# Optimization experiments

Hardware: AMD Instinct MI355X
Metric: run time of the kernel (lower is better)

Reference implementation:

```python
import jax, jax.numpy as jnp
import numpy as np

N, D, K, A, BINS, DEPTH = 1024, 384, 64, 5, 64, 4
D_MAX = 22.0


def _expected_distance(distogram):
    # distance_one_hot_inverse(softmax(distogram), 0.0, 22.0, 64)
    step = D_MAX / BINS
    centers = step * jnp.arange(BINS, dtype=distogram.dtype) + step / 2
    p = jax.nn.softmax(distogram, axis=-1)  # [N,N,BINS]
    return (p * centers).sum(axis=-1)       # [N,N]


def _extract_neighbours(pos, prev_pos, distogram, resi, chain, batch, mask, key):
    inf = jnp.inf
    same_batch = batch[:, None] == batch[None, :]
    same_chain = (chain[:, None] == chain[None, :]) & same_batch
    pair_mask = mask[:, None] & mask[None, :] & same_batch
    # sequence-separation distance (only within a chain), 3.81 A per residue
    seq_d = jnp.where(same_chain,
                      jnp.abs(resi[:, None] - resi[None, :]).astype(jnp.float32) * 3.81,
                      inf)
    md = _expected_distance(distogram)
    d = jnp.minimum(seq_d, jnp.where(md < 8.0, md, inf))
    ca = pos[:, 1]                                   # current CA positions [N,3]
    d = jnp.minimum(d, jnp.linalg.norm(ca[:, None] - ca[None, :], axis=-1))
    pca = prev_pos[:, 1]
    d = jnp.minimum(d, jnp.linalg.norm(pca[:, None] - pca[None, :], axis=-1))
    d = jnp.where(same_batch, d, inf)
    log_p = -3.0 * d
    u = jax.random.uniform(key, d.shape)
    gumbel = -jnp.log(-jnp.log(u + 1e-6) + 1e-6)
    random_distance = -(log_p + gumbel)
    random_distance = jnp.where(pair_mask, random_distance, inf)
    neg_vals, idx = jax.lax.top_k(-random_distance, K)  # k smallest random distances
    nbr_mask = jnp.isfinite(neg_vals)                   # invalid neighbours have -inf
    return idx, nbr_mask                                # [N,K] int32, [N,K] bool


def setup_inputs() -> dict:
    key = jax.random.key(0)
    ks = jax.random.split(key, 8)
    local = jax.random.normal(ks[0], (N, D), dtype=jnp.float32)
    pos = 3.0 * jax.random.normal(ks[1], (N, A, 3), dtype=jnp.float32)
    prev_pos = 3.0 * jax.random.normal(ks[2], (N, A, 3), dtype=jnp.float32)
    distogram = jax.random.normal(ks[3], (N, N, BINS), dtype=jnp.float32)
    Wn = jax.random.normal(ks[4], (D, D), dtype=jnp.float32) / np.sqrt(D)
    Wp = 0.01 * jax.random.normal(ks[5], (D, A * 3), dtype=jnp.float32)
    ar = jnp.arange(N, dtype=jnp.int32)
    batch = ar // 256          # 4 proteins of 256 residues
    chain = (ar // 128) % 2    # 2 chains per protein
    resi = ar % 128            # residue index within chain
    mask = jnp.ones((N,), dtype=bool)
    return {"local": local, "pos": pos, "prev_pos": prev_pos, "distogram": distogram,
            "Wn": Wn, "Wp": Wp, "resi": resi, "chain": chain, "batch": batch, "mask": mask}


def reference(local, pos, prev_pos, distogram, Wn, Wp, resi, chain, batch, mask):
    mask_f = mask.astype(local.dtype)
    key = jax.random.key(42)
    traj = []
    for t in range(DEPTH):  # diffusion_depth iterations, neighbours recomputed each block
        idx, nbr_mask = _extract_neighbours(pos, prev_pos, distogram, resi, chain,
                                            batch, mask, jax.random.fold_in(key, t))
        nf = local[idx] * nbr_mask[..., None].astype(local.dtype)   # [N,K,D]
        cnt = jnp.maximum(nbr_mask.sum(axis=1, keepdims=True).astype(local.dtype), 1.0)
        msg = nf.sum(axis=1) / cnt                                   # [N,D]
        local = local + jax.nn.gelu(msg @ Wn)
        pos = pos + 0.1 * (local @ Wp).reshape(N, A, 3) * mask_f[:, None, None]
        traj.append(pos)
    trajectory = jnp.stack(traj)  # [DEPTH,N,A,3]
    return local, pos, trajectory
```

## Files before the change

kernel.cpp:

```cpp
#include <hip/hip_runtime.h>
#include <stdint.h>

typedef unsigned int u32;
typedef unsigned long long u64;

#define NN 1024
#define DDIM 384
#define KNB 64
#define BINS_ 64
#define DEPTH_ 4

#define OUT_POS 393216
#define OUT_TRAJ 408576

__device__ __forceinline__ u32 rotl32(u32 x, int r) { return (x << r) | (x >> (32 - r)); }

__device__ __forceinline__ void threefry(u32 k0, u32 k1, u32 x0, u32 x1, u32& o0, u32& o1) {
  u32 ks2 = k0 ^ k1 ^ 0x1BD11BDAu;
#define TF_R(r) { x0 += x1; x1 = rotl32(x1, r); x1 ^= x0; }
  x0 += k0; x1 += k1;
  TF_R(13) TF_R(15) TF_R(26) TF_R(6)
  x0 += k1; x1 += ks2 + 1u;
  TF_R(17) TF_R(29) TF_R(16) TF_R(24)
  x0 += ks2; x1 += k0 + 2u;
  TF_R(13) TF_R(15) TF_R(26) TF_R(6)
  x0 += k0; x1 += k1 + 3u;
  TF_R(17) TF_R(29) TF_R(16) TF_R(24)
  x0 += k1; x1 += ks2 + 4u;
  TF_R(13) TF_R(15) TF_R(26) TF_R(6)
  x0 += ks2; x1 += k0 + 5u;
#undef TF_R
  o0 = x0; o1 = x1;
}

static inline u32 h_rotl32(u32 x, int r) { return (x << r) | (x >> (32 - r)); }
static void h_threefry(u32 k0, u32 k1, u32 x0, u32 x1, u32& o0, u32& o1) {
  u32 ks2 = k0 ^ k1 ^ 0x1BD11BDAu;
#define TF_R(r) { x0 += x1; x1 = h_rotl32(x1, r); x1 ^= x0; }
  x0 += k0; x1 += k1;
  TF_R(13) TF_R(15) TF_R(26) TF_R(6)
  x0 += k1; x1 += ks2 + 1u;
  TF_R(17) TF_R(29) TF_R(16) TF_R(24)
  x0 += ks2; x1 += k0 + 2u;
  TF_R(13) TF_R(15) TF_R(26) TF_R(6)
  x0 += k0; x1 += k1 + 3u;
  TF_R(17) TF_R(29) TF_R(16) TF_R(24)
  x0 += k1; x1 += ks2 + 4u;
  TF_R(13) TF_R(15) TF_R(26) TF_R(6)
  x0 += ks2; x1 += k0 + 5u;
#undef TF_R
  o0 = x0; o1 = x1;
}

__global__ __launch_bounds__(256) void k_dstatic(
    const float* __restrict__ disto, const float* __restrict__ ppos,
    const int* __restrict__ resi, const int* __restrict__ chain,
    const int* __restrict__ batch, float* __restrict__ dstat) {
  int p = blockIdx.x * 256 + threadIdx.x;
  int i = p >> 10, j = p & 1023;
  if (batch[i] != batch[j]) { dstat[p] = __builtin_inff(); return; }
  float seq_d = __builtin_inff();
  if (chain[i] == chain[j]) {
    int dr = resi[i] - resi[j];
    seq_d = __fmul_rn(fabsf((float)dr), 3.81f);
  }
  const float4* dp = reinterpret_cast<const float4*>(disto + (size_t)p * BINS_);
  float w[BINS_];
#pragma unroll
  for (int q = 0; q < 16; ++q) {
    float4 v = dp[q];
    w[4*q+0] = v.x; w[4*q+1] = v.y; w[4*q+2] = v.z; w[4*q+3] = v.w;
  }
  float m = -__builtin_inff();
#pragma unroll
  for (int q = 0; q < BINS_; ++q) m = fmaxf(m, w[q]);
  float s = 0.f;
#pragma unroll
  for (int q = 0; q < BINS_; ++q) {
    w[q] = expf(__fsub_rn(w[q], m));
    s = __fadd_rn(s, w[q]);
  }
  float e = 0.f;
#pragma unroll
  for (int q = 0; q < BINS_; ++q) {
    float pq = __fdiv_rn(w[q], s);
    e = __fadd_rn(e, __fmul_rn(pq, 0.34375f * (float)q + 0.171875f));
  }
  float md = e;
  float d = fminf(seq_d, (md < 8.0f) ? md : __builtin_inff());
  float ax = __fsub_rn(ppos[i*15+3], ppos[j*15+3]);
  float ay = __fsub_rn(ppos[i*15+4], ppos[j*15+4]);
  float az = __fsub_rn(ppos[i*15+5], ppos[j*15+5]);
  float ss = __fadd_rn(__fadd_rn(__fmul_rn(ax,ax), __fmul_rn(ay,ay)), __fmul_rn(az,az));
  dstat[p] = fminf(d, __fsqrt_rn(ss));
}

__device__ __forceinline__ u64 shx64(u64 x, int m) {
  int lo = __shfl_xor((int)(u32)x, m, 64);
  int hi = __shfl_xor((int)(u32)(x >> 32), m, 64);
  return ((u64)(u32)hi << 32) | (u32)lo;
}

__device__ __forceinline__ u64 merge64(u64 a, u64 b, int lane) {
  u64 br = shx64(b, 63);
  u64 m = (a < br) ? a : br;
  for (int stride = 32; stride > 0; stride >>= 1) {
    u64 p = shx64(m, stride);
    u64 lo = (m < p) ? m : p;
    u64 hi = (m < p) ? p : m;
    m = ((lane & stride) == 0) ? lo : hi;
  }
  return m;
}

__global__ __launch_bounds__(384) void k_round(
    const float* __restrict__ dstat, const float* __restrict__ Lprev,
    float* __restrict__ Lnext, const float* __restrict__ posP,
    float* __restrict__ posN, const int* __restrict__ batch,
    const float* __restrict__ Wn, const float* __restrict__ Wp,
    float* __restrict__ out, int t, u32 fk0, u32 fk1) {
  __shared__ int sidx[4][KNB];
  __shared__ float cntL[4];
  __shared__ float msgT[4][DDIM];
  __shared__ float lrT[4][DDIM + 1];
  const int tid = threadIdx.x;
  const int w = tid >> 6, lane = tid & 63;
  const int i0 = blockIdx.x * 4;

  if (w < 4) {
    const int i = i0 + w;
    const int bi = batch[i];
    const float cax = posP[i*15+3], cay = posP[i*15+4], caz = posP[i*15+5];
    u64 v[16];
#pragma unroll
    for (int c = 0; c < 16; ++c) {
      int j = c*64 + lane;
      float rd = __builtin_inff();
      if (batch[j] == bi) {
        float d = dstat[i*NN + j];
        float dx = __fsub_rn(cax, posP[j*15+3]);
        float dy = __fsub_rn(cay, posP[j*15+4]);
        float dz = __fsub_rn(caz, posP[j*15+5]);
        float ss = __fadd_rn(__fadd_rn(__fmul_rn(dx,dx), __fmul_rn(dy,dy)), __fmul_rn(dz,dz));
        d = fminf(d, __fsqrt_rn(ss));
        u32 o0, o1;
        threefry(fk0, fk1, 0u, (u32)(i*NN + j), o0, o1);
        u32 bits = o0 ^ o1;
        float u = __fsub_rn(__uint_as_float((bits >> 9) | 0x3f800000u), 1.0f);
        float inner = __fadd_rn(-logf(__fadd_rn(u, 1e-6f)), 1e-6f);
        float gum = -logf(inner);
        float logp = __fmul_rn(-3.0f, d);
        rd = -__fadd_rn(logp, gum);
      }
      u32 fb = __float_as_uint(rd);
      u32 km = (fb & 0x80000000u) ? ~fb : (fb | 0x80000000u);
      v[c] = ((u64)km << 32) | (u32)j;
    }
    for (int size = 2; size <= 64; size <<= 1) {
      for (int stride = size >> 1; stride > 0; stride >>= 1) {
        bool keepmin = (((lane & stride) == 0) == ((lane & size) == 0));
#pragma unroll
        for (int c = 0; c < 16; ++c) {
          u64 p = shx64(v[c], stride);
          u64 lo = (v[c] < p) ? v[c] : p;
          u64 hi = (v[c] < p) ? p : v[c];
          v[c] = keepmin ? lo : hi;
        }
      }
    }
#pragma unroll
    for (int c = 0; c < 8; ++c) v[c] = merge64(v[2*c], v[2*c+1], lane);
#pragma unroll
    for (int c = 0; c < 4; ++c) v[c] = merge64(v[2*c], v[2*c+1], lane);
#pragma unroll
    for (int c = 0; c < 2; ++c) v[c] = merge64(v[2*c], v[2*c+1], lane);
    u64 m = merge64(v[0], v[1], lane);
    u32 km = (u32)(m >> 32);
    bool fin = (km < 0xFF800000u);
    sidx[w][lane] = fin ? (int)(u32)(m & 0xffffffffu) : -1;
    u64 ball = __ballot(fin);
    if (lane == 0) cntL[w] = fmaxf((float)__popcll(ball), 1.0f);
  }
  __syncthreads();

  {
    const int c = tid;
#pragma unroll
    for (int r = 0; r < 4; ++r) {
      float s = 0.f;
#pragma unroll 8
      for (int k = 0; k < KNB; ++k) {
        int id = sidx[r][k];
        if (id >= 0) s += Lprev[id*DDIM + c];
      }
      msgT[r][c] = s / cntL[r];
    }
  }
  __syncthreads();

  {
    const int c = tid;
    float a0 = 0.f, a1 = 0.f, a2 = 0.f, a3 = 0.f;
#pragma unroll 8
    for (int dd = 0; dd < DDIM; ++dd) {
      float wv = Wn[dd*DDIM + c];
      a0 = fmaf(msgT[0][dd], wv, a0);
      a1 = fmaf(msgT[1][dd], wv, a1);
      a2 = fmaf(msgT[2][dd], wv, a2);
      a3 = fmaf(msgT[3][dd], wv, a3);
    }
    float accs[4] = {a0, a1, a2, a3};
#pragma unroll
    for (int r = 0; r < 4; ++r) {
      float x = accs[r];
      float th = tanhf(0.7978845608028654f * (x + 0.044715f * x * x * x));
      float g = 0.5f * x * (1.0f + th);
      float ln = Lprev[(i0 + r)*DDIM + c] + g;
      Lnext[(i0 + r)*DDIM + c] = ln;
      lrT[r][c] = ln;
    }
  }
  __syncthreads();

  if (tid < 60) {
    const int r = tid / 15, cc = tid % 15;
    const int i = i0 + r;
    float acc = 0.f;
#pragma unroll 8
    for (int dd = 0; dd < DDIM; ++dd) acc = fmaf(lrT[r][dd], Wp[dd*15 + cc], acc);
    float pv = posP[i*15 + cc] + 0.1f * acc;
    posN[i*15 + cc] = pv;
    out[OUT_TRAJ + t*15360 + i*15 + cc] = pv;
  }
}

extern "C" void kernel_launch(void* const* d_in, const int* in_sizes, int n_in,
                              void* d_out, int out_size, void* d_ws, size_t ws_size,
                              hipStream_t stream) {
  (void)in_sizes; (void)n_in; (void)out_size; (void)ws_size;
  const float* local_in = (const float*)d_in[0];
  const float* pos_in   = (const float*)d_in[1];
  const float* ppos_in  = (const float*)d_in[2];
  const float* disto    = (const float*)d_in[3];
  const float* Wn       = (const float*)d_in[4];
  const float* Wp       = (const float*)d_in[5];
  const int* resi       = (const int*)d_in[6];
  const int* chain      = (const int*)d_in[7];
  const int* batch      = (const int*)d_in[8];
  float* out = (float*)d_out;
  char* ws = (char*)d_ws;
  float* dstat = (float*)(ws + 0);
  float* L0    = (float*)(ws + 4194304);
  float* L1    = (float*)(ws + 5767168);
  float* P0    = (float*)(ws + 7340032);
  float* P1    = (float*)(ws + 7401472);

  k_dstatic<<<dim3(4096), dim3(256), 0, stream>>>(disto, ppos_in, resi, chain, batch, dstat);

  const float* Lp = local_in;
  const float* Pp = pos_in;
  float* Lbuf[2] = {L0, L1};
  float* Pbuf[2] = {P0, P1};
  for (int t = 0; t < DEPTH_; ++t) {
    u32 fk0, fk1;
    h_threefry(0u, 42u, 0u, (u32)t, fk0, fk1);
    float* Ln = (t == DEPTH_ - 1) ? out : Lbuf[t & 1];
    float* Pn = (t == DEPTH_ - 1) ? (out + OUT_POS) : Pbuf[t & 1];
    k_round<<<dim3(256), dim3(384), 0, stream>>>(dstat, Lp, Ln, Pp, Pn, batch,
                                                 Wn, Wp, out, t, fk0, fk1);
    Lp = Ln; Pp = Pn;
  }
}
```

Measured before the change: 687.8 us.

## Split top-k selection from gather/matmul and skip sorting chunks outside the batch

Each round is split into two kernels. A one-wave-per-row top-k kernel runs on 1024 blocks and skips the bitonic sort and merges for 64-column chunks that hold no same-batch entries. A separate gather/matmul/update kernel then handles 2 rows per block across 512 blocks. The aim is more parallelism than the previous 256 blocks, where only 4 of 6 waves did the top-k, and less wasted sorting of all-infinite chunks. The cost is an extra launch per round and an index/count round trip through global memory, and each Wn column is now loaded for 2 rows instead of 4.

```diff
diff --git a/kernel.cpp b/kernel.cpp
--- a/kernel.cpp
+++ b/kernel.cpp
@@ -101,6 +101,19 @@
   return ((u64)(u32)hi << 32) | (u32)lo;
 }
 
+__device__ __forceinline__ u64 sort64(u64 x, int lane) {
+  for (int size = 2; size <= 64; size <<= 1) {
+    for (int stride = size >> 1; stride > 0; stride >>= 1) {
+      bool keepmin = (((lane & stride) == 0) == ((lane & size) == 0));
+      u64 p = shx64(x, stride);
+      u64 lo = (x < p) ? x : p;
+      u64 hi = (x < p) ? p : x;
+      x = keepmin ? lo : hi;
+    }
+  }
+  return x;
+}
+
 __device__ __forceinline__ u64 merge64(u64 a, u64 b, int lane) {
   u64 br = shx64(b, 63);
   u64 m = (a < br) ? a : br;
@@ -113,105 +126,129 @@
   return m;
 }
 
-__global__ __launch_bounds__(384) void k_round(
-    const float* __restrict__ dstat, const float* __restrict__ Lprev,
-    float* __restrict__ Lnext, const float* __restrict__ posP,
-    float* __restrict__ posN, const int* __restrict__ batch,
+__global__ __launch_bounds__(64) void k_topk(
+    const float* __restrict__ dstat, const float* __restrict__ posP,
+    const int* __restrict__ batch, int* __restrict__ idx,
+    float* __restrict__ cntv, u32 fk0, u32 fk1) {
+  const int i = blockIdx.x;
+  const int lane = threadIdx.x;
+  const int bi = batch[i];
+  const float cax = posP[i*15+3], cay = posP[i*15+4], caz = posP[i*15+5];
+  u64 v[16];
+  unsigned vmask = 0;
+#pragma unroll
+  for (int c = 0; c < 16; ++c) {
+    int j = c*64 + lane;
+    bool sb = (batch[j] == bi);
+    if (__ballot(sb) != 0ull) vmask |= (1u << c);
+    float rd = __builtin_inff();
+    if (sb) {
+      float d = dstat[i*NN + j];
+      float dx = __fsub_rn(cax, posP[j*15+3]);
+      float dy = __fsub_rn(cay, posP[j*15+4]);
+      float dz = __fsub_rn(caz, posP[j*15+5]);
+      float ss = __fadd_rn(__fadd_rn(__fmul_rn(dx,dx), __fmul_rn(dy,dy)), __fmul_rn(dz,dz));
+      d = fminf(d, __fsqrt_rn(ss));
+      u32 o0, o1;
+      threefry(fk0, fk1, 0u, (u32)(i*NN + j), o0, o1);
+      u32 bits = o0 ^ o1;
+      float u = __fsub_rn(__uint_as_float((bits >> 9) | 0x3f800000u), 1.0f);
+      float inner = __fadd_rn(-logf(__fadd_rn(u, 1e-6f)), 1e-6f);
+      float gum = -logf(inner);
+      float logp = __fmul_rn(-3.0f, d);
+      rd = -__fadd_rn(logp, gum);
+    }
+    u32 fb = __float_as_uint(rd);
+    u32 km = (fb & 0x80000000u) ? ~fb : (fb | 0x80000000u);
+    v[c] = ((u64)km << 32) | (u32)j;
+  }
+#pragma unroll
+  for (int c = 0; c < 16; ++c)
+    if (vmask & (1u << c)) v[c] = sort64(v[c], lane);
+  u64 m1[8]; unsigned vm1 = 0;
+#pragma unroll
+  for (int c = 0; c < 8; ++c) {
+    bool va = (vmask >> (2*c)) & 1u, vb = (vmask >> (2*c+1)) & 1u;
+    u64 r = 0;
+    if (va && vb) r = merge64(v[2*c], v[2*c+1], lane);
+    else if (va) r = v[2*c];
+    else if (vb) r = v[2*c+1];
+    m1[c] = r; vm1 |= (u32)(va || vb) << c;
+  }
+  u64 m2[4]; unsigned vm2 = 0;
+#pragma unroll
+  for (int c = 0; c < 4; ++c) {
+    bool va = (vm1 >> (2*c)) & 1u, vb = (vm1 >> (2*c+1)) & 1u;
+    u64 r = 0;
+    if (va && vb) r = merge64(m1[2*c], m1[2*c+1], lane);
+    else if (va) r = m1[2*c];
+    else if (vb) r = m1[2*c+1];
+    m2[c] = r; vm2 |= (u32)(va || vb) << c;
+  }
+  u64 m3[2]; unsigned vm3 = 0;
+#pragma unroll
+  for (int c = 0; c < 2; ++c) {
+    bool va = (vm2 >> (2*c)) & 1u, vb = (vm2 >> (2*c+1)) & 1u;
+    u64 r = 0;
+    if (va && vb) r = merge64(m2[2*c], m2[2*c+1], lane);
+    else if (va) r = m2[2*c];
+    else if (vb) r = m2[2*c+1];
+    m3[c] = r; vm3 |= (u32)(va || vb) << c;
+  }
+  u64 m;
+  {
+    bool va = vm3 & 1u, vb = (vm3 >> 1) & 1u;
+    if (va && vb) m = merge64(m3[0], m3[1], lane);
+    else if (va) m = m3[0];
+    else if (vb) m = m3[1];
+    else m = ((u64)0xFF800000u << 32) | (u32)lane;
+  }
+  u32 km = (u32)(m >> 32);
+  bool fin = (km < 0xFF800000u);
+  idx[i*KNB + lane] = fin ? (int)(u32)(m & 0xffffffffu) : -1;
+  u64 ball = __ballot(fin);
+  if (lane == 0) cntv[i] = fmaxf((float)__popcll(ball), 1.0f);
+}
+
+__global__ __launch_bounds__(384) void k_gmu(
+    const float* __restrict__ Lprev, float* __restrict__ Lnext,
+    const float* __restrict__ posP, float* __restrict__ posN,
+    const int* __restrict__ idx, const float* __restrict__ cntv,
     const float* __restrict__ Wn, const float* __restrict__ Wp,
-    float* __restrict__ out, int t, u32 fk0, u32 fk1) {
-  __shared__ int sidx[4][KNB];
-  __shared__ float cntL[4];
-  __shared__ float msgT[4][DDIM];
-  __shared__ float lrT[4][DDIM + 1];
+    float* __restrict__ out, int t) {
+  __shared__ int sidx[2][KNB];
+  __shared__ float msgT[2][DDIM];
+  __shared__ float lrT[2][DDIM + 1];
   const int tid = threadIdx.x;
-  const int w = tid >> 6, lane = tid & 63;
-  const int i0 = blockIdx.x * 4;
-
-  if (w < 4) {
-    const int i = i0 + w;
-    const int bi = batch[i];
-    const float cax = posP[i*15+3], cay = posP[i*15+4], caz = posP[i*15+5];
-    u64 v[16];
-#pragma unroll
-    for (int c = 0; c < 16; ++c) {
-      int j = c*64 + lane;
-      float rd = __builtin_inff();
-      if (batch[j] == bi) {
-        float d = dstat[i*NN + j];
-        float dx = __fsub_rn(cax, posP[j*15+3]);
-        float dy = __fsub_rn(cay, posP[j*15+4]);
-        float dz = __fsub_rn(caz, posP[j*15+5]);
-        float ss = __fadd_rn(__fadd_rn(__fmul_rn(dx,dx), __fmul_rn(dy,dy)), __fmul_rn(dz,dz));
-        d = fminf(d, __fsqrt_rn(ss));
-        u32 o0, o1;
-        threefry(fk0, fk1, 0u, (u32)(i*NN + j), o0, o1);
-        u32 bits = o0 ^ o1;
-        float u = __fsub_rn(__uint_as_float((bits >> 9) | 0x3f800000u), 1.0f);
-        float inner = __fadd_rn(-logf(__fadd_rn(u, 1e-6f)), 1e-6f);
-        float gum = -logf(inner);
-        float logp = __fmul_rn(-3.0f, d);
-        rd = -__fadd_rn(logp, gum);
-      }
-      u32 fb = __float_as_uint(rd);
-      u32 km = (fb & 0x80000000u) ? ~fb : (fb | 0x80000000u);
-      v[c] = ((u64)km << 32) | (u32)j;
-    }
-    for (int size = 2; size <= 64; size <<= 1) {
-      for (int stride = size >> 1; stride > 0; stride >>= 1) {
-        bool keepmin = (((lane & stride) == 0) == ((lane & size) == 0));
-#pragma unroll
-        for (int c = 0; c < 16; ++c) {
-          u64 p = shx64(v[c], stride);
-          u64 lo = (v[c] < p) ? v[c] : p;
-          u64 hi = (v[c] < p) ? p : v[c];
-          v[c] = keepmin ? lo : hi;
-        }
-      }
-    }
-#pragma unroll
-    for (int c = 0; c < 8; ++c) v[c] = merge64(v[2*c], v[2*c+1], lane);
-#pragma unroll
-    for (int c = 0; c < 4; ++c) v[c] = merge64(v[2*c], v[2*c+1], lane);
-#pragma unroll
-    for (int c = 0; c < 2; ++c) v[c] = merge64(v[2*c], v[2*c+1], lane);
-    u64 m = merge64(v[0], v[1], lane);
-    u32 km = (u32)(m >> 32);
-    bool fin = (km < 0xFF800000u);
-    sidx[w][lane] = fin ? (int)(u32)(m & 0xffffffffu) : -1;
-    u64 ball = __ballot(fin);
-    if (lane == 0) cntL[w] = fmaxf((float)__popcll(ball), 1.0f);
-  }
+  const int i0 = blockIdx.x * 2;
+  if (tid < 2*KNB) sidx[tid >> 6][tid & 63] = idx[(i0 + (tid >> 6))*KNB + (tid & 63)];
   __syncthreads();
-
   {
     const int c = tid;
 #pragma unroll
-    for (int r = 0; r < 4; ++r) {
+    for (int r = 0; r < 2; ++r) {
       float s = 0.f;
 #pragma unroll 8
       for (int k = 0; k < KNB; ++k) {
         int id = sidx[r][k];
         if (id >= 0) s += Lprev[id*DDIM + c];
       }
-      msgT[r][c] = s / cntL[r];
+      msgT[r][c] = s / cntv[i0 + r];
     }
   }
   __syncthreads();
-
   {
     const int c = tid;
-    float a0 = 0.f, a1 = 0.f, a2 = 0.f, a3 = 0.f;
+    float a0 = 0.f, a1 = 0.f;
 #pragma unroll 8
     for (int dd = 0; dd < DDIM; ++dd) {
       float wv = Wn[dd*DDIM + c];
       a0 = fmaf(msgT[0][dd], wv, a0);
       a1 = fmaf(msgT[1][dd], wv, a1);
-      a2 = fmaf(msgT[2][dd], wv, a2);
-      a3 = fmaf(msgT[3][dd], wv, a3);
-    }
-    float accs[4] = {a0, a1, a2, a3};
-#pragma unroll
-    for (int r = 0; r < 4; ++r) {
+    }
+    float accs[2] = {a0, a1};
+#pragma unroll
+    for (int r = 0; r < 2; ++r) {
       float x = accs[r];
       float th = tanhf(0.7978845608028654f * (x + 0.044715f * x * x * x));
       float g = 0.5f * x * (1.0f + th);
@@ -221,8 +258,7 @@
     }
   }
   __syncthreads();
-
-  if (tid < 60) {
+  if (tid < 30) {
     const int r = tid / 15, cc = tid % 15;
     const int i = i0 + r;
     float acc = 0.f;
@@ -254,6 +290,8 @@
   float* L1    = (float*)(ws + 5767168);
   float* P0    = (float*)(ws + 7340032);
   float* P1    = (float*)(ws + 7401472);
+  int*   idxb  = (int*)(ws + 7462912);
+  float* cntb  = (float*)(ws + 7725056);
 
   k_dstatic<<<dim3(4096), dim3(256), 0, stream>>>(disto, ppos_in, resi, chain, batch, dstat);
 
@@ -266,8 +304,8 @@
     h_threefry(0u, 42u, 0u, (u32)t, fk0, fk1);
     float* Ln = (t == DEPTH_ - 1) ? out : Lbuf[t & 1];
     float* Pn = (t == DEPTH_ - 1) ? (out + OUT_POS) : Pbuf[t & 1];
-    k_round<<<dim3(256), dim3(384), 0, stream>>>(dstat, Lp, Ln, Pp, Pn, batch,
-                                                 Wn, Wp, out, t, fk0, fk1);
+    k_topk<<<dim3(NN), dim3(64), 0, stream>>>(dstat, Pp, batch, idxb, cntb, fk0, fk1);
+    k_gmu<<<dim3(512), dim3(384), 0, stream>>>(Lp, Ln, Pp, Pn, idxb, cntb, Wn, Wp, out, t);
     Lp = Ln; Pp = Pn;
   }
 }
```

After: 596.0 us. 13.3% less time.
